# Kernel tuning notes

Measured on AMD Instinct MI355X. Metric: run time of the kernel, lower is better.

The kernel has to match this reference:

```python
import jax, jax.numpy as jnp
import numpy as np

T = 16384  # sequence length (scan axis)
D = 512    # d_model


def setup_inputs() -> dict:
    key = jax.random.key(0)
    k1, k2, k3, k4 = jax.random.split(key, 4)
    inputs = jax.random.normal(k1, (T, D), dtype=jnp.float32)
    terminations = jax.random.bernoulli(k2, 0.01, (T,))
    c0 = jnp.zeros((D,), dtype=jnp.float32)
    h0 = jnp.zeros((D,), dtype=jnp.float32)
    # flax OptimizedLSTMCell fuses the 4 gates (order i, f, g, o) into one kernel
    scale = 1.0 / np.sqrt(D).astype(np.float32)
    Wx = jax.random.normal(k3, (D, 4 * D), dtype=jnp.float32) * scale  # input kernel (no bias in flax)
    Wh = jax.random.normal(k4, (D, 4 * D), dtype=jnp.float32) * scale  # recurrent kernel
    b = jnp.zeros((4 * D,), dtype=jnp.float32)                          # recurrent-dense bias
    return {"inputs": inputs, "terminations": terminations, "c0": c0, "h0": h0,
            "Wx": Wx, "Wh": Wh, "b": b}


def reference(inputs, terminations, c0, h0, Wx, Wh, b):
    def step(carry, xt):
        x, term = xt
        c, h = carry
        # reset_on_terminate: zero the carry when this step begins a new episode
        keep = jnp.where(term, jnp.zeros((), c.dtype), jnp.ones((), c.dtype))
        c = c * keep
        h = h * keep
        # fused gate pre-activations, flax gate order: i, f, g, o
        z = x @ Wx + h @ Wh + b  # [4*D]
        i, f, g, o = jnp.split(z, 4, axis=-1)
        new_c = jax.nn.sigmoid(f) * c + jax.nn.sigmoid(i) * jnp.tanh(g)
        new_h = jax.nn.sigmoid(o) * jnp.tanh(new_c)
        return (new_c, new_h), (new_c, new_h)

    _, (cs, hs) = jax.lax.scan(step, (c0, h0), (inputs, terminations))
    # original returns (y_t, new_states) with y_t == new_h per step -> (hs, (cs, hs))
    return hs, cs, hs
```

## Files before the change

kernel.cpp:

```cpp
#include <hip/hip_runtime.h>

typedef _Float16 half8 __attribute__((ext_vector_type(8)));
typedef float floatx4 __attribute__((ext_vector_type(4)));
typedef unsigned int u32x4 __attribute__((ext_vector_type(4)));
typedef unsigned long long u64;
typedef unsigned int u32;
typedef unsigned short u16;

#define T_LEN 16384
#define DM 512
#define NC 2048
#define NG 16
#define NR 16
#define WPG 16
#define WVG 32

struct Meta { int S; int use_h0; int steps_g[NG]; };

union FragU { u64 q[2]; u32x4 r; half8 v; };

__device__ __forceinline__ float sigf(float x) { return 1.0f / (1.0f + __expf(-x)); }
__device__ __forceinline__ float tanh_f(float x) { return 1.0f - 2.0f / (__expf(2.0f * x) + 1.0f); }

__global__ void zero_kernel(u32* __restrict__ p, size_t nwords) {
    size_t i = (size_t)blockIdx.x * blockDim.x + threadIdx.x;
    size_t stride = (size_t)gridDim.x * blockDim.x;
    for (; i < nwords; i += stride) p[i] = 0u;
}

__global__ void pack_f16_kernel(const float* __restrict__ src, _Float16* __restrict__ dst, int n8) {
    int i = blockIdx.x * blockDim.x + threadIdx.x;
    if (i >= n8) return;
    const floatx4* s = (const floatx4*)src + (size_t)i * 2;
    floatx4 a = s[0], b = s[1];
    half8 o;
    o[0] = (_Float16)a[0]; o[1] = (_Float16)a[1]; o[2] = (_Float16)a[2]; o[3] = (_Float16)a[3];
    o[4] = (_Float16)b[0]; o[5] = (_Float16)b[1]; o[6] = (_Float16)b[2]; o[7] = (_Float16)b[3];
    ((half8*)dst)[i] = o;
}

__global__ __launch_bounds__(256) void pack_w_kernel(const float* __restrict__ src, half8* __restrict__ dst) {
    int wid = blockIdx.x * 4 + (threadIdx.x >> 6);
    int l = threadIdx.x & 63;
    int tt = wid >> 4, kt = wid & 15;
    int q = tt & 3, cch = tt >> 2;
    int col = q * 512 + cch * 16 + (l & 15);
    int h = l >> 4;
    half8 o;
#pragma unroll
    for (int jj = 0; jj < 8; jj++) o[jj] = (_Float16)src[(size_t)(kt * 32 + h * 8 + jj) * NC + col];
    dst[(tt * 16 + kt) * 64 + l] = o;
}

__global__ void prep_kernel(const void* __restrict__ termraw, const float* __restrict__ h0,
                            int* __restrict__ seg_start, int* __restrict__ seg_len,
                            Meta* __restrict__ meta, _Float16* __restrict__ Hbuf) {
    __shared__ int cnts[256], offs[256];
    __shared__ int nzm, oddnz, totS;
    __shared__ int chain[256];
    int tid = threadIdx.x;
    if (tid == 0) { nzm = 0; oddnz = 0; }
    __syncthreads();
    const unsigned char* tb = (const unsigned char*)termraw;
    const int* ti = (const int*)termraw;
    int lm = 0;
    for (int i = tid; i < T_LEN; i += 256) {
        if (tb[i]) {
            int p = i & 3;
            if (p == 1 || p == 2) lm |= 1;
            else if (p == 3) lm |= 2;
            else lm |= 4;
        }
    }
    if (lm) atomicOr(&nzm, lm);
    __syncthreads();
    int mm = nzm;
    int bytemode = (mm & 1) ? 1 : 0;
    int floatmode = (!bytemode && (mm & 2)) ? 1 : 0;
    int lo = 0;
    if (!bytemode && !floatmode) {
        for (int k2 = 2 * tid + 1; k2 < T_LEN; k2 += 512) if (ti[k2]) lo = 1;
    }
    if (lo) atomicOr(&oddnz, 1);
    __syncthreads();
    int i64mode = (!bytemode && !floatmode && oddnz == 0 && (mm & 4)) ? 1 : 0;
    const float* tf = (const float*)termraw;

    auto termAt = [&](int t) -> int {
        if (bytemode) return tb[t] != 0;
        if (floatmode) return tf[t] != 0.0f;
        if (i64mode) return (ti[2 * t] != 0) || (ti[2 * t + 1] != 0);
        return ti[t] != 0;
    };

    int base = tid * 64;
    int cnt = 0;
    for (int k = 0; k < 64; k++) {
        int t = base + k;
        if (t == 0 || termAt(t)) cnt++;
    }
    cnts[tid] = cnt;
    __syncthreads();
    if (tid == 0) {
        int a = 0;
        for (int i = 0; i < 256; i++) { offs[i] = a; a += cnts[i]; }
        totS = a;
        meta->S = a;
    }
    __syncthreads();
    int S = totS;
    {
        int o = offs[tid];
        for (int k = 0; k < 64; k++) {
            int t = base + k;
            if (t == 0 || termAt(t)) seg_start[o++] = t;
        }
    }
    __syncthreads();
    for (int i = tid; i < S; i += 256)
        seg_len[i] = ((i + 1 < S) ? seg_start[i + 1] : T_LEN) - seg_start[i];
    __syncthreads();
    {
        int g = tid >> 4, r = tid & 15;
        int tot = 0;
        for (int i = g + 16 * r; i < S; i += 256) tot += seg_len[i];
        chain[tid] = tot;
    }
    __syncthreads();
    if (tid < NG) {
        int mx = 0;
        for (int r = 0; r < 16; r++) mx = max(mx, chain[tid * 16 + r]);
        meta->steps_g[tid] = mx;
    }
    int u = termAt(0);
    if (tid == 0) meta->use_h0 = !u;
    if (!u) {
        for (int d2 = tid; d2 < DM; d2 += 256)
            Hbuf[(d2 >> 3) * 128 + (d2 & 7)] = (_Float16)h0[d2];
    }
}

__global__ __launch_bounds__(256) void xw_gemm_kernel(const half8* __restrict__ A, const half8* __restrict__ B,
                                                      const float* __restrict__ bias, _Float16* __restrict__ XW) {
    int bx = blockIdx.x, by = blockIdx.y;
    int w = threadIdx.x >> 6, l = threadIdx.x & 63;
    int mbase = bx * 64 + w * 16;
    int h = l >> 4, n = l & 15;
    floatx4 acc[8] = {};
    int arow = mbase + n;
#pragma unroll
    for (int kt = 0; kt < 16; kt++) {
        half8 a = A[(size_t)arow * 64 + kt * 4 + h];
#pragma unroll
        for (int nt = 0; nt < 8; nt++)
            acc[nt] = __builtin_amdgcn_mfma_f32_16x16x32_f16(a, B[((by * 8 + nt) * 16 + kt) * 64 + l], acc[nt], 0, 0, 0);
    }
#pragma unroll
    for (int nt = 0; nt < 8; nt++) {
        int tt = by * 8 + nt, q = tt & 3, cch = tt >> 2;
        float bv = bias[q * 512 + cch * 16 + n];
#pragma unroll
        for (int r = 0; r < 4; r++) {
            int row = mbase + h * 4 + r;
            XW[(size_t)row * NC + tt * 16 + n] = (_Float16)(acc[nt][r] + bv);
        }
    }
}

struct Trk { int seg, t0, s0, end, active; };

__device__ __forceinline__ void trk_init(Trk& k, int row, int g, int S,
                                         const int* __restrict__ ss, const int* __restrict__ sl) {
    int seg = g + 16 * row;
    k.seg = seg;
    if (seg < S) { k.t0 = ss[seg]; k.s0 = 0; k.end = sl[seg]; k.active = 1; }
    else { k.t0 = 0; k.s0 = 0; k.end = 0x7fffffff; k.active = 0; }
}

__device__ __forceinline__ int trk_step(Trk& k, int s, int S,
                                        const int* __restrict__ ss, const int* __restrict__ sl, int& t_out) {
    int z = !k.active;
    if (s > 0 && k.active && s == k.end) {
        int seg = k.seg + 256;
        if (seg < S) { k.seg = seg; k.t0 = ss[seg]; k.s0 = s; k.end = s + sl[seg]; z = 1; }
        else { k.active = 0; z = 1; }
    }
    t_out = k.active ? (k.t0 + (s - k.s0)) : 0;
    return z;
}

__global__ __launch_bounds__(128, 1) void scan_kernel(
    const half8* __restrict__ PW, const _Float16* __restrict__ XW,
    const float* __restrict__ c0,
    const int* __restrict__ seg_start, const int* __restrict__ seg_len,
    const Meta* __restrict__ meta,
    u64* __restrict__ Hbuf, int* __restrict__ flags,
    float* __restrict__ out) {
    const int b = blockIdx.x;
    const int g = (b & 7) * 2 + (b >> 7);
    const int jj = (b >> 3) & 15;
    const int tid = threadIdx.x;
    const int w = tid >> 6, l = tid & 63;
    const int c = jj * 2 + w;
    const int S = meta->S;
    const int steps = meta->steps_g[g];
    if (steps <= 0) return;
    const int use_h0 = meta->use_h0;
    const int n = l & 15, h = l >> 4;
    const int d = c * 16 + n;

    __shared__ __align__(16) u16 hstage[2][NR][16];

    half8 bf[4][16];
#pragma unroll
    for (int q = 0; q < 4; q++)
#pragma unroll
        for (int kt = 0; kt < 16; kt++) {
            bf[q][kt] = PW[((c * 4 + q) * 16 + kt) * 64 + l];
            asm volatile("" : "+v"(bf[q][kt]));
        }

    Trk trkM; trk_init(trkM, n, g, S, seg_start, seg_len);
    Trk trk[4];
#pragma unroll
    for (int r = 0; r < 4; r++) trk_init(trk[r], h * 4 + r, g, S, seg_start, seg_len);

    float cc[4];
#pragma unroll
    for (int r = 0; r < 4; r++) {
        int row = h * 4 + r;
        cc[r] = (g == 0 && row == 0 && use_h0) ? c0[d] : 0.0f;
    }

    FragU zu; zu.q[0] = 0; zu.q[1] = 0;
    const half8 zfrag = zu.v;

    int* fl = flags + g * WVG;
    const int wfid = jj * 2 + w;
    const int pollidx = l & 31;

    float* outH = out;
    float* outC = out + (size_t)T_LEN * DM;
    float* outH2 = out + 2 * (size_t)T_LEN * DM;

    const int b2 = l >> 5, m2 = (l >> 1) & 15, half = l & 1;
    const int ktc = c >> 1, hhp = (c & 1) * 2 + b2;
    const int ldsIdx = m2 * 4 + b2 * 2 + half;
    const size_t hwIdx = (size_t)(ktc * 4 + hhp) * 32 + m2 * 2 + half;

    int tdump;
    int zM = trk_step(trkM, 0, S, seg_start, seg_len, tdump);
    int zz[4], tr[4], act[4];
#pragma unroll
    for (int r = 0; r < 4; r++) {
        zz[r] = trk_step(trk[r], 0, S, seg_start, seg_len, tr[r]);
        act[r] = trk[r].active;
    }
    float xwv[4][4];
#pragma unroll
    for (int q = 0; q < 4; q++)
#pragma unroll
        for (int r = 0; r < 4; r++)
            xwv[q][r] = (float)XW[(size_t)tr[r] * NC + (c * 4 + q) * 16 + n];

    for (int s = 0; s < steps; ++s) {
        if (s > 0) {
            while (true) {
                int v = __hip_atomic_load(&fl[pollidx], __ATOMIC_RELAXED, __HIP_MEMORY_SCOPE_AGENT);
                if (__all(v >= s)) break;
                __builtin_amdgcn_s_sleep(1);
            }
            asm volatile("" ::: "memory");
        }

        const int rp = s & 1;
        u64* Hr = Hbuf + (size_t)(g * 2 + rp) * (NR * DM / 4);
        u64* Hw = Hbuf + (size_t)(g * 2 + (rp ^ 1)) * (NR * DM / 4);

        const int m = n;
        u32x4 raw[16];
#pragma unroll
        for (int kt = 0; kt < 16; kt++) {
            const void* ap = (const char*)Hr + (((size_t)kt * 64 + h * 16 + m) << 4);
            asm volatile("global_load_dwordx4 %0, %1, off sc1" : "=v"(raw[kt]) : "v"(ap) : "memory");
        }
        asm volatile("s_waitcnt vmcnt(0)" ::: "memory");
        __builtin_amdgcn_sched_barrier(0);
        half8 afr[16];
#pragma unroll
        for (int kt = 0; kt < 16; kt++) {
            FragU u; u.r = raw[kt];
            afr[kt] = zM ? zfrag : u.v;
        }

        floatx4 acc[4] = {};
#pragma unroll
        for (int kt = 0; kt < 16; kt++) {
#pragma unroll
            for (int q = 0; q < 4; q++)
                acc[q] = __builtin_amdgcn_mfma_f32_16x16x32_f16(afr[kt], bf[q][kt], acc[q], 0, 0, 0);
        }

        float hnv[4], cnv[4];
#pragma unroll
        for (int r = 0; r < 4; r++) {
            float zi = acc[0][r] + xwv[0][r];
            float zf = acc[1][r] + xwv[1][r];
            float zg = acc[2][r] + xwv[2][r];
            float zo = acc[3][r] + xwv[3][r];
            float cprev = zz[r] ? 0.0f : cc[r];
            float cn = sigf(zf) * cprev + sigf(zi) * tanh_f(zg);
            float hn = sigf(zo) * tanh_f(cn);
            cc[r] = cn; hnv[r] = hn; cnv[r] = cn;
            hstage[w][h * 4 + r][n] = __builtin_bit_cast(u16, (_Float16)hn);
        }

        asm volatile("s_waitcnt lgkmcnt(0)" ::: "memory");
        __builtin_amdgcn_sched_barrier(0);
        u64 pk = ((const u64*)&hstage[w][0][0])[ldsIdx];
        __hip_atomic_store(&Hw[hwIdx], pk, __ATOMIC_RELAXED, __HIP_MEMORY_SCOPE_AGENT);

        asm volatile("s_waitcnt vmcnt(0)" ::: "memory");
        if (l == 0)
            __hip_atomic_store(&fl[wfid], s + 1, __ATOMIC_RELAXED, __HIP_MEMORY_SCOPE_AGENT);

        int otr[4], oact[4];
#pragma unroll
        for (int r = 0; r < 4; r++) { otr[r] = tr[r]; oact[r] = act[r]; }

        zM = trk_step(trkM, s + 1, S, seg_start, seg_len, tdump);
#pragma unroll
        for (int r = 0; r < 4; r++) {
            zz[r] = trk_step(trk[r], s + 1, S, seg_start, seg_len, tr[r]);
            act[r] = trk[r].active;
        }
#pragma unroll
        for (int q = 0; q < 4; q++)
#pragma unroll
            for (int r = 0; r < 4; r++)
                xwv[q][r] = (float)XW[(size_t)tr[r] * NC + (c * 4 + q) * 16 + n];

#pragma unroll
        for (int r = 0; r < 4; r++) {
            if (oact[r]) {
                size_t oo = (size_t)otr[r] * DM + d;
                outH[oo] = hnv[r]; outC[oo] = cnv[r]; outH2[oo] = hnv[r];
            }
        }
    }
}

extern "C" void kernel_launch(void* const* d_in, const int* in_sizes, int n_in,
                              void* d_out, int out_size, void* d_ws, size_t ws_size,
                              hipStream_t stream) {
    const float* inputs = (const float*)d_in[0];
    const void* terms = d_in[1];
    const float* c0 = (const float*)d_in[2];
    const float* h0 = (const float*)d_in[3];
    const float* Wx = (const float*)d_in[4];
    const float* Wh = (const float*)d_in[5];
    const float* bias = (const float*)d_in[6];
    float* out = (float*)d_out;

    size_t off = 0;
    auto take = [&](size_t bts) { size_t cur = off; off = (off + bts + 255) & ~(size_t)255; return cur; };
    size_t offXW = take((size_t)T_LEN * NC * 2);
    size_t offAin = take((size_t)T_LEN * DM * 2);
    size_t offPX = take((size_t)DM * NC * 2);
    size_t offPW = take((size_t)DM * NC * 2);
    size_t offSS = take((size_t)(T_LEN + 2) * 4);
    size_t offSL = take((size_t)(T_LEN + 2) * 4);
    size_t offH = take(2ull * NG * NR * DM * 2);
    size_t offFL = take((size_t)NG * WVG * 4);
    size_t offME = take(256);
    size_t total = off;
    (void)ws_size;

    char* W = (char*)d_ws;
    _Float16* Ain = (_Float16*)(W + offAin);
    half8* PX = (half8*)(W + offPX);
    half8* PWp = (half8*)(W + offPW);
    int* segS = (int*)(W + offSS);
    int* segL = (int*)(W + offSL);
    Meta* meta = (Meta*)(W + offME);
    _Float16* XWp = (_Float16*)(W + offXW);

    size_t zwords = (total - offH) / 4;
    zero_kernel<<<256, 256, 0, stream>>>((u32*)(W + offH), zwords);
    pack_f16_kernel<<<(T_LEN * DM / 8 + 255) / 256, 256, 0, stream>>>(inputs, Ain, T_LEN * DM / 8);
    pack_w_kernel<<<512, 256, 0, stream>>>(Wx, PX);
    pack_w_kernel<<<512, 256, 0, stream>>>(Wh, PWp);
    prep_kernel<<<1, 256, 0, stream>>>(terms, h0, segS, segL, meta, (_Float16*)(W + offH));

    dim3 gg(T_LEN / 64, NC / 128);
    xw_gemm_kernel<<<gg, 256, 0, stream>>>((const half8*)Ain, (const half8*)PX, bias, XWp);
    scan_kernel<<<256, 128, 0, stream>>>((const half8*)PWp, XWp, c0, segS, segL, meta,
                                         (u64*)(W + offH), (int*)(W + offFL), out);
}
```

Before: 2.086 ms.

## Add producer/consumer I/O wavefront to prefetch XW and drain outputs

Adds a third wavefront per block that prefetches the precomputed input-projection rows into double-buffered LDS and writes the h/c outputs to global memory with vectorised stores. The two compute wavefronts now only read gate inputs from LDS and stage results there, signalling through LDS flags. The aim is to take global loads and scattered output stores off the latency-critical recurrent step. In exchange it adds intra-block spin-waits and LDS traffic, and the compute waves can stall if the I/O wave falls behind.

```diff
diff --git a/kernel.cpp b/kernel.cpp
--- a/kernel.cpp
+++ b/kernel.cpp
@@ -189,7 +189,7 @@
     return z;
 }
 
-__global__ __launch_bounds__(128, 1) void scan_kernel(
+__global__ __launch_bounds__(192, 1) void scan_kernel(
     const half8* __restrict__ PW, const _Float16* __restrict__ XW,
     const float* __restrict__ c0,
     const int* __restrict__ seg_start, const int* __restrict__ seg_len,
@@ -201,151 +201,210 @@
     const int jj = (b >> 3) & 15;
     const int tid = threadIdx.x;
     const int w = tid >> 6, l = tid & 63;
-    const int c = jj * 2 + w;
     const int S = meta->S;
     const int steps = meta->steps_g[g];
     if (steps <= 0) return;
     const int use_h0 = meta->use_h0;
-    const int n = l & 15, h = l >> 4;
-    const int d = c * 16 + n;
 
     __shared__ __align__(16) u16 hstage[2][NR][16];
-
-    half8 bf[4][16];
-#pragma unroll
-    for (int q = 0; q < 4; q++)
-#pragma unroll
-        for (int kt = 0; kt < 16; kt++) {
-            bf[q][kt] = PW[((c * 4 + q) * 16 + kt) * 64 + l];
-            asm volatile("" : "+v"(bf[q][kt]));
-        }
-
-    Trk trkM; trk_init(trkM, n, g, S, seg_start, seg_len);
-    Trk trk[4];
-#pragma unroll
-    for (int r = 0; r < 4; r++) trk_init(trk[r], h * 4 + r, g, S, seg_start, seg_len);
-
-    float cc[4];
-#pragma unroll
-    for (int r = 0; r < 4; r++) {
-        int row = h * 4 + r;
-        cc[r] = (g == 0 && row == 0 && use_h0) ? c0[d] : 0.0f;
-    }
-
-    FragU zu; zu.q[0] = 0; zu.q[1] = 0;
-    const half8 zfrag = zu.v;
-
-    int* fl = flags + g * WVG;
-    const int wfid = jj * 2 + w;
-    const int pollidx = l & 31;
+    __shared__ __align__(16) _Float16 xwstage[2][NR][128];
+    __shared__ __align__(16) float outstage[2][2][NR][32];
+    __shared__ int ioflag[2];
+    __shared__ int outcnt[2];
+
+    if (tid == 0) { ioflag[0] = -1; ioflag[1] = -1; outcnt[0] = 0; outcnt[1] = 0; }
+    __syncthreads();
 
     float* outH = out;
     float* outC = out + (size_t)T_LEN * DM;
     float* outH2 = out + 2 * (size_t)T_LEN * DM;
 
-    const int b2 = l >> 5, m2 = (l >> 1) & 15, half = l & 1;
-    const int ktc = c >> 1, hhp = (c & 1) * 2 + b2;
-    const int ldsIdx = m2 * 4 + b2 * 2 + half;
-    const size_t hwIdx = (size_t)(ktc * 4 + hhp) * 32 + m2 * 2 + half;
-
-    int tdump;
-    int zM = trk_step(trkM, 0, S, seg_start, seg_len, tdump);
-    int zz[4], tr[4], act[4];
-#pragma unroll
-    for (int r = 0; r < 4; r++) {
-        zz[r] = trk_step(trk[r], 0, S, seg_start, seg_len, tr[r]);
-        act[r] = trk[r].active;
-    }
-    float xwv[4][4];
-#pragma unroll
-    for (int q = 0; q < 4; q++)
-#pragma unroll
-        for (int r = 0; r < 4; r++)
-            xwv[q][r] = (float)XW[(size_t)tr[r] * NC + (c * 4 + q) * 16 + n];
-
-    for (int s = 0; s < steps; ++s) {
-        if (s > 0) {
-            while (true) {
-                int v = __hip_atomic_load(&fl[pollidx], __ATOMIC_RELAXED, __HIP_MEMORY_SCOPE_AGENT);
-                if (__all(v >= s)) break;
+    if (w < 2) {
+        const int c = jj * 2 + w;
+        const int n = l & 15, h = l >> 4;
+        const int d = c * 16 + n;
+
+        half8 bf[4][16];
+#pragma unroll
+        for (int q = 0; q < 4; q++)
+#pragma unroll
+            for (int kt = 0; kt < 16; kt++) {
+                bf[q][kt] = PW[((c * 4 + q) * 16 + kt) * 64 + l];
+                asm volatile("" : "+v"(bf[q][kt]));
+            }
+
+        Trk trkM; trk_init(trkM, n, g, S, seg_start, seg_len);
+        Trk trk[4];
+#pragma unroll
+        for (int r = 0; r < 4; r++) trk_init(trk[r], h * 4 + r, g, S, seg_start, seg_len);
+
+        float cc[4];
+#pragma unroll
+        for (int r = 0; r < 4; r++) {
+            int row = h * 4 + r;
+            cc[r] = (g == 0 && row == 0 && use_h0) ? c0[d] : 0.0f;
+        }
+
+        FragU zu; zu.q[0] = 0; zu.q[1] = 0;
+        const half8 zfrag = zu.v;
+
+        int* fl = flags + g * WVG;
+        const int wfid = jj * 2 + w;
+        const int pollidx = l & 31;
+
+        const int b2 = l >> 5, m2 = (l >> 1) & 15, half = l & 1;
+        const int ktc = c >> 1, hhp = (c & 1) * 2 + b2;
+        const int ldsIdx = m2 * 4 + b2 * 2 + half;
+        const size_t hwIdx = (size_t)(ktc * 4 + hhp) * 32 + m2 * 2 + half;
+
+        for (int s = 0; s < steps; ++s) {
+            int tdump;
+            const int zM = trk_step(trkM, s, S, seg_start, seg_len, tdump);
+            int zz[4];
+#pragma unroll
+            for (int r = 0; r < 4; r++)
+                zz[r] = trk_step(trk[r], s, S, seg_start, seg_len, tdump);
+
+            while (__hip_atomic_load(&ioflag[s & 1], __ATOMIC_RELAXED, __HIP_MEMORY_SCOPE_WORKGROUP) < s)
                 __builtin_amdgcn_s_sleep(1);
-            }
             asm volatile("" ::: "memory");
-        }
-
-        const int rp = s & 1;
-        u64* Hr = Hbuf + (size_t)(g * 2 + rp) * (NR * DM / 4);
-        u64* Hw = Hbuf + (size_t)(g * 2 + (rp ^ 1)) * (NR * DM / 4);
-
-        const int m = n;
-        u32x4 raw[16];
-#pragma unroll
-        for (int kt = 0; kt < 16; kt++) {
-            const void* ap = (const char*)Hr + (((size_t)kt * 64 + h * 16 + m) << 4);
-            asm volatile("global_load_dwordx4 %0, %1, off sc1" : "=v"(raw[kt]) : "v"(ap) : "memory");
-        }
-        asm volatile("s_waitcnt vmcnt(0)" ::: "memory");
-        __builtin_amdgcn_sched_barrier(0);
-        half8 afr[16];
-#pragma unroll
-        for (int kt = 0; kt < 16; kt++) {
-            FragU u; u.r = raw[kt];
-            afr[kt] = zM ? zfrag : u.v;
-        }
-
-        floatx4 acc[4] = {};
-#pragma unroll
-        for (int kt = 0; kt < 16; kt++) {
+            float xwv[4][4];
 #pragma unroll
             for (int q = 0; q < 4; q++)
-                acc[q] = __builtin_amdgcn_mfma_f32_16x16x32_f16(afr[kt], bf[q][kt], acc[q], 0, 0, 0);
-        }
-
-        float hnv[4], cnv[4];
-#pragma unroll
-        for (int r = 0; r < 4; r++) {
-            float zi = acc[0][r] + xwv[0][r];
-            float zf = acc[1][r] + xwv[1][r];
-            float zg = acc[2][r] + xwv[2][r];
-            float zo = acc[3][r] + xwv[3][r];
-            float cprev = zz[r] ? 0.0f : cc[r];
-            float cn = sigf(zf) * cprev + sigf(zi) * tanh_f(zg);
-            float hn = sigf(zo) * tanh_f(cn);
-            cc[r] = cn; hnv[r] = hn; cnv[r] = cn;
-            hstage[w][h * 4 + r][n] = __builtin_bit_cast(u16, (_Float16)hn);
-        }
-
-        asm volatile("s_waitcnt lgkmcnt(0)" ::: "memory");
-        __builtin_amdgcn_sched_barrier(0);
-        u64 pk = ((const u64*)&hstage[w][0][0])[ldsIdx];
-        __hip_atomic_store(&Hw[hwIdx], pk, __ATOMIC_RELAXED, __HIP_MEMORY_SCOPE_AGENT);
-
-        asm volatile("s_waitcnt vmcnt(0)" ::: "memory");
-        if (l == 0)
-            __hip_atomic_store(&fl[wfid], s + 1, __ATOMIC_RELAXED, __HIP_MEMORY_SCOPE_AGENT);
-
-        int otr[4], oact[4];
-#pragma unroll
-        for (int r = 0; r < 4; r++) { otr[r] = tr[r]; oact[r] = act[r]; }
-
-        zM = trk_step(trkM, s + 1, S, seg_start, seg_len, tdump);
-#pragma unroll
-        for (int r = 0; r < 4; r++) {
-            zz[r] = trk_step(trk[r], s + 1, S, seg_start, seg_len, tr[r]);
-            act[r] = trk[r].active;
-        }
-#pragma unroll
-        for (int q = 0; q < 4; q++)
-#pragma unroll
-            for (int r = 0; r < 4; r++)
-                xwv[q][r] = (float)XW[(size_t)tr[r] * NC + (c * 4 + q) * 16 + n];
-
-#pragma unroll
-        for (int r = 0; r < 4; r++) {
-            if (oact[r]) {
-                size_t oo = (size_t)otr[r] * DM + d;
-                outH[oo] = hnv[r]; outC[oo] = cnv[r]; outH2[oo] = hnv[r];
-            }
+#pragma unroll
+                for (int r = 0; r < 4; r++)
+                    xwv[q][r] = (float)xwstage[s & 1][h * 4 + r][w * 64 + q * 16 + n];
+
+            if (s > 0) {
+                while (true) {
+                    int v = __hip_atomic_load(&fl[pollidx], __ATOMIC_RELAXED, __HIP_MEMORY_SCOPE_AGENT);
+                    if (__all(v >= s)) break;
+                    __builtin_amdgcn_s_sleep(1);
+                }
+                asm volatile("" ::: "memory");
+            }
+
+            const int rp = s & 1;
+            u64* Hr = Hbuf + (size_t)(g * 2 + rp) * (NR * DM / 4);
+            u64* Hw = Hbuf + (size_t)(g * 2 + (rp ^ 1)) * (NR * DM / 4);
+
+            const int m = n;
+            u32x4 raw[16];
+#pragma unroll
+            for (int kt = 0; kt < 16; kt++) {
+                const void* ap = (const char*)Hr + (((size_t)kt * 64 + h * 16 + m) << 4);
+                asm volatile("global_load_dwordx4 %0, %1, off sc1" : "=v"(raw[kt]) : "v"(ap) : "memory");
+            }
+            asm volatile("s_waitcnt vmcnt(0)" ::: "memory");
+            __builtin_amdgcn_sched_barrier(0);
+            half8 afr[16];
+#pragma unroll
+            for (int kt = 0; kt < 16; kt++) {
+                FragU u; u.r = raw[kt];
+                afr[kt] = zM ? zfrag : u.v;
+            }
+
+            floatx4 acc[4] = {};
+#pragma unroll
+            for (int kt = 0; kt < 16; kt++) {
+#pragma unroll
+                for (int q = 0; q < 4; q++)
+                    acc[q] = __builtin_amdgcn_mfma_f32_16x16x32_f16(afr[kt], bf[q][kt], acc[q], 0, 0, 0);
+            }
+
+            float hnv[4], cnv[4];
+#pragma unroll
+            for (int r = 0; r < 4; r++) {
+                float zi = acc[0][r] + xwv[0][r];
+                float zf = acc[1][r] + xwv[1][r];
+                float zg = acc[2][r] + xwv[2][r];
+                float zo = acc[3][r] + xwv[3][r];
+                float cprev = zz[r] ? 0.0f : cc[r];
+                float cn = sigf(zf) * cprev + sigf(zi) * tanh_f(zg);
+                float hn = sigf(zo) * tanh_f(cn);
+                cc[r] = cn; hnv[r] = hn; cnv[r] = cn;
+                hstage[w][h * 4 + r][n] = __builtin_bit_cast(u16, (_Float16)hn);
+            }
+
+            asm volatile("s_waitcnt lgkmcnt(0)" ::: "memory");
+            __builtin_amdgcn_sched_barrier(0);
+            u64 pk = ((const u64*)&hstage[w][0][0])[ldsIdx];
+            __hip_atomic_store(&Hw[hwIdx], pk, __ATOMIC_RELAXED, __HIP_MEMORY_SCOPE_AGENT);
+
+            asm volatile("s_waitcnt vmcnt(0)" ::: "memory");
+            if (l == 0)
+                __hip_atomic_store(&fl[wfid], s + 1, __ATOMIC_RELAXED, __HIP_MEMORY_SCOPE_AGENT);
+
+            while (__hip_atomic_load(&outcnt[s & 1], __ATOMIC_RELAXED, __HIP_MEMORY_SCOPE_WORKGROUP) == 2)
+                __builtin_amdgcn_s_sleep(1);
+            asm volatile("" ::: "memory");
+#pragma unroll
+            for (int r = 0; r < 4; r++) {
+                outstage[s & 1][0][h * 4 + r][w * 16 + n] = hnv[r];
+                outstage[s & 1][1][h * 4 + r][w * 16 + n] = cnv[r];
+            }
+            asm volatile("s_waitcnt lgkmcnt(0)" ::: "memory");
+            if (l == 0)
+                __hip_atomic_fetch_add(&outcnt[s & 1], 1, __ATOMIC_RELAXED, __HIP_MEMORY_SCOPE_WORKGROUP);
+        }
+    } else {
+        const int rX = l >> 4;
+        const int rO = l >> 3;
+        Trk trkX[4];
+#pragma unroll
+        for (int i = 0; i < 4; i++) trk_init(trkX[i], rX + 4 * i, g, S, seg_start, seg_len);
+        Trk trkO[2];
+        trk_init(trkO[0], rO, g, S, seg_start, seg_len);
+        trk_init(trkO[1], rO + 8, g, S, seg_start, seg_len);
+
+        auto stageXW = [&](int step, int buf) {
+            int tX[4], td;
+#pragma unroll
+            for (int i = 0; i < 4; i++) (void)trk_step(trkX[i], step, S, seg_start, seg_len, tX[i]);
+            u32x4 xr[4];
+#pragma unroll
+            for (int i = 0; i < 4; i++)
+                xr[i] = *(const u32x4*)((const char*)XW + ((size_t)tX[i] * NC + jj * 128 + (l & 15) * 8) * 2);
+            (void)td;
+#pragma unroll
+            for (int i = 0; i < 4; i++)
+                *(u32x4*)&xwstage[buf][rX + 4 * i][(l & 15) * 8] = xr[i];
+            asm volatile("s_waitcnt lgkmcnt(0)" ::: "memory");
+            if (l == 0)
+                __hip_atomic_store(&ioflag[buf], step, __ATOMIC_RELAXED, __HIP_MEMORY_SCOPE_WORKGROUP);
+        };
+
+        stageXW(0, 0);
+        stageXW(1, 1);
+
+        for (int s = 0; s < steps; ++s) {
+            int tO[2], aO[2];
+#pragma unroll
+            for (int j2 = 0; j2 < 2; j2++) {
+                (void)trk_step(trkO[j2], s, S, seg_start, seg_len, tO[j2]);
+                aO[j2] = trkO[j2].active;
+            }
+            while (__hip_atomic_load(&outcnt[s & 1], __ATOMIC_RELAXED, __HIP_MEMORY_SCOPE_WORKGROUP) < 2)
+                __builtin_amdgcn_s_sleep(1);
+            asm volatile("" ::: "memory");
+            floatx4 hv[2], cv[2];
+#pragma unroll
+            for (int j2 = 0; j2 < 2; j2++) {
+                hv[j2] = *(floatx4*)&outstage[s & 1][0][rO + 8 * j2][(l & 7) * 4];
+                cv[j2] = *(floatx4*)&outstage[s & 1][1][rO + 8 * j2][(l & 7) * 4];
+            }
+            asm volatile("s_waitcnt lgkmcnt(0)" ::: "memory");
+            __hip_atomic_store(&outcnt[s & 1], 0, __ATOMIC_RELAXED, __HIP_MEMORY_SCOPE_WORKGROUP);
+#pragma unroll
+            for (int j2 = 0; j2 < 2; j2++) {
+                if (aO[j2]) {
+                    size_t base = (size_t)tO[j2] * DM + jj * 32 + (l & 7) * 4;
+                    *(floatx4*)&outH[base] = hv[j2];
+                    *(floatx4*)&outC[base] = cv[j2];
+                    *(floatx4*)&outH2[base] = hv[j2];
+                }
+            }
+            stageXW(s + 2, s & 1);
         }
     }
 }
@@ -394,6 +453,6 @@
 
     dim3 gg(T_LEN / 64, NC / 128);
     xw_gemm_kernel<<<gg, 256, 0, stream>>>((const half8*)Ain, (const half8*)PX, bias, XWp);
-    scan_kernel<<<256, 128, 0, stream>>>((const half8*)PWp, XWp, c0, segS, segL, meta,
+    scan_kernel<<<256, 192, 0, stream>>>((const half8*)PWp, XWp, c0, segS, segL, meta,
                                          (u64*)(W + offH), (int*)(W + offFL), out);
 }
```

Result: faster. 1.799 ms (-13.8%).
